# Kernel optimization log

Measured on AMD Instinct MI355X. Metric: run time of the kernel, lower is better.

Reference implementation:

```python
import jax, jax.numpy as jnp
import numpy as np

EPS = 1e-6
B, T, C = 2, 1024, 2048
H, KV, D = 32, 8, 128
E, F, TOPK = 8, 768, 2


def rmsnorm(x, w):
    xf = x.astype(jnp.float32)
    var = jnp.mean(xf * xf, axis=-1, keepdims=True)
    return w * (xf * jax.lax.rsqrt(var + EPS)).astype(x.dtype)


def rotate_half(x):
    d = x.shape[-1] // 2
    return jnp.concatenate([-x[..., d:], x[..., :d]], axis=-1)


def setup_inputs() -> dict:
    key = jax.random.key(0)
    ks = jax.random.split(key, 12)
    sc = 0.02
    x = jax.random.normal(ks[0], (B, T, C), dtype=jnp.float32)
    # RoPE tables: cos/sin of shape [B, T, D]
    inv_freq = 1.0 / (1e6 ** (np.arange(0, D, 2, dtype=np.float32) / D))
    pos = np.arange(T, dtype=np.float32)
    freqs = pos[:, None] * inv_freq[None, :]          # [T, D/2]
    emb = np.concatenate([freqs, freqs], axis=-1)     # [T, D]
    cos = jnp.broadcast_to(jnp.cos(emb)[None], (B, T, D)).astype(jnp.float32)
    sin = jnp.broadcast_to(jnp.sin(emb)[None], (B, T, D)).astype(jnp.float32)
    return {
        "x": x, "cos": cos, "sin": sin,
        "ln1_w": jnp.ones((C,), jnp.float32),
        "q_w": jax.random.normal(ks[1], (C, H * D), jnp.float32) * sc,
        "k_w": jax.random.normal(ks[2], (C, KV * D), jnp.float32) * sc,
        "v_w": jax.random.normal(ks[3], (C, KV * D), jnp.float32) * sc,
        "o_w": jax.random.normal(ks[4], (H * D, C), jnp.float32) * sc,
        "qn_w": jnp.ones((D,), jnp.float32),
        "kn_w": jnp.ones((D,), jnp.float32),
        "ln2_w": jnp.ones((C,), jnp.float32),
        "gate_w": jax.random.normal(ks[5], (C, E), jnp.float32) * sc,
        "gate_up_w": jax.random.normal(ks[6], (E, C, 2 * F), jnp.float32) * sc,
        "down_w": jax.random.normal(ks[7], (E, F, C), jnp.float32) * sc,
    }


def reference(x, cos, sin, ln1_w, q_w, k_w, v_w, o_w, qn_w, kn_w, ln2_w,
              gate_w, gate_up_w, down_w):
    b, t, c = x.shape
    # ---- attention branch ----
    h = rmsnorm(x, ln1_w)
    q = (h @ q_w).reshape(b, t, H, D)
    k = (h @ k_w).reshape(b, t, KV, D)
    v = (h @ v_w).reshape(b, t, KV, D)
    q = rmsnorm(q, qn_w)
    k = rmsnorm(k, kn_w)
    cb = cos[:, :, None, :]
    sb = sin[:, :, None, :]
    q = q * cb + rotate_half(q) * sb
    k = k * cb + rotate_half(k) * sb
    rep = H // KV
    k = jnp.repeat(k, rep, axis=2)  # [b,t,H,D]
    v = jnp.repeat(v, rep, axis=2)
    scores = jnp.einsum('bthd,bshd->bhts', q, k) / jnp.sqrt(jnp.float32(D))
    causal = jnp.tril(jnp.ones((t, t), dtype=bool))
    scores = jnp.where(causal, scores, jnp.finfo(scores.dtype).min)
    attn = jax.nn.softmax(scores, axis=-1)
    ao = jnp.einsum('bhts,bshd->bthd', attn, v).reshape(b, t, H * D) @ o_w
    x = x + ao
    # ---- MoE branch ----
    h2 = rmsnorm(x, ln2_w)
    hidden = h2.reshape(-1, c)                     # [N, C]
    logits = hidden @ gate_w                       # [N, E]
    rw = jax.nn.softmax(logits.astype(jnp.float32), axis=-1)
    tw, ti = jax.lax.top_k(rw, TOPK)
    tw = tw / (tw.sum(axis=-1, keepdims=True) + 1e-9)
    n = hidden.shape[0]
    routed = jnp.zeros_like(logits).at[jnp.arange(n)[:, None], ti].set(tw.astype(logits.dtype))
    routed = routed / (routed.sum(axis=-1, keepdims=True) + 1e-9)
    gu = jnp.einsum('th,ehq->teq', hidden, gate_up_w)   # [N, E, 2F]
    g, u = jnp.split(gu, 2, axis=-1)
    eo = jnp.einsum('teq,eqh->teh', jax.nn.silu(g) * u, down_w)  # [N, E, C]
    moe = (eo * routed[..., None]).sum(axis=1).reshape(b, t, c)
    return x + moe
```

## Files before the change

kernel.cpp:

```cpp
#include <hip/hip_runtime.h>
#include <hip/hip_bf16.h>

typedef short bf16x8 __attribute__((ext_vector_type(8)));
typedef float f32x4 __attribute__((ext_vector_type(4)));
typedef unsigned short u16;

#define NTOK 2048
#define CDIM 2048
#define TSEQ 1024
#define NH   32
#define NKV  8
#define DH   128
#define NE   8
#define FDIM 768
#define CAP  2048

#define GLOAD_LDS16(g, l) \
  __builtin_amdgcn_global_load_lds((const __attribute__((address_space(1))) void*)(g), \
                                   (__attribute__((address_space(3))) void*)(l), 16, 0, 0)

__device__ __forceinline__ u16 f2bf(float f){
  union { float f; unsigned u; } v; v.f = f;
  unsigned r = v.u + 0x7FFFu + ((v.u >> 16) & 1u);
  return (u16)(r >> 16);
}
__device__ __forceinline__ float bf2f(u16 x){
  union { unsigned u; float f; } v; v.u = ((unsigned)x) << 16; return v.f;
}

__device__ __forceinline__ f32x4 mfma_bf16(bf16x8 a, bf16x8 b, f32x4 c){
  return __builtin_amdgcn_mfma_f32_16x16x32_bf16(a, b, c, 0, 0, 0);
}

__device__ __forceinline__ int xcd_swz(int orig, int nwg){
  int xcd = orig & 7;
  int q = nwg >> 3, r = nwg & 7;
  int base = (xcd < r) ? xcd*(q+1) : r*(q+1) + (xcd-r)*q;
  return base + (orig >> 3);
}

__global__ void cast_transpose(const float* __restrict__ in, u16* __restrict__ out,
                               int R, int Cc, int rstride, int d1,
                               long long s_hi, long long s_lo)
{
  __shared__ u16 tile[64][72];
  int z = blockIdx.z;
  in  += (long long)(z / d1) * s_hi + (long long)(z % d1) * s_lo;
  out += (size_t)z * R * Cc;
  int r0 = blockIdx.y*64, c0 = blockIdx.x*64;
  int lr = threadIdx.x >> 4;
  int lc = (threadIdx.x & 15) * 4;
  #pragma unroll
  for(int i=0;i<4;i++){
    int r = lr + i*16;
    float4 v = *(const float4*)(in + (size_t)(r0 + r)*rstride + c0 + lc);
    tile[lc+0][r] = f2bf(v.x);
    tile[lc+1][r] = f2bf(v.y);
    tile[lc+2][r] = f2bf(v.z);
    tile[lc+3][r] = f2bf(v.w);
  }
  __syncthreads();
  int oc  = threadIdx.x >> 2;
  int orr = (threadIdx.x & 3) * 16;
  uint4 a  = *(const uint4*)&tile[oc][orr];
  uint4 b2 = *(const uint4*)&tile[oc][orr + 8];
  *(uint4*)(out + (size_t)(c0+oc)*R + r0 + orr)     = a;
  *(uint4*)(out + (size_t)(c0+oc)*R + r0 + orr + 8) = b2;
}

__global__ void cast_transpose_qkv(const float* __restrict__ qw, const float* __restrict__ kw,
                                   const float* __restrict__ vw, u16* __restrict__ wqkvT)
{
  __shared__ u16 tile[64][72];
  int bx = blockIdx.x;
  const float* in; u16* out; int rstride, c0;
  if(bx < 64){       in = qw; out = wqkvT;                        rstride = 4096; c0 = bx*64; }
  else if(bx < 80){  in = kw; out = wqkvT + (size_t)4096*2048;    rstride = 1024; c0 = (bx-64)*64; }
  else {             in = vw; out = wqkvT + (size_t)5120*2048;    rstride = 1024; c0 = (bx-80)*64; }
  const int R = 2048;
  int r0 = blockIdx.y*64;
  int lr = threadIdx.x >> 4;
  int lc = (threadIdx.x & 15) * 4;
  #pragma unroll
  for(int i=0;i<4;i++){
    int r = lr + i*16;
    float4 v = *(const float4*)(in + (size_t)(r0 + r)*rstride + c0 + lc);
    tile[lc+0][r] = f2bf(v.x);
    tile[lc+1][r] = f2bf(v.y);
    tile[lc+2][r] = f2bf(v.z);
    tile[lc+3][r] = f2bf(v.w);
  }
  __syncthreads();
  int oc  = threadIdx.x >> 2;
  int orr = (threadIdx.x & 3) * 16;
  uint4 a  = *(const uint4*)&tile[oc][orr];
  uint4 b2 = *(const uint4*)&tile[oc][orr + 8];
  *(uint4*)(out + (size_t)(c0+oc)*R + r0 + orr)     = a;
  *(uint4*)(out + (size_t)(c0+oc)*R + r0 + orr + 8) = b2;
}

__global__ void transpose_gate(const float* __restrict__ gw, float* __restrict__ gwT)
{
  int i = blockIdx.x*256 + threadIdx.x;
  int c = i >> 3, e = i & 7;
  gwT[(size_t)e*CDIM + c] = gw[(size_t)c*NE + e];
}

__global__ void transpose_u16(const u16* __restrict__ in, u16* __restrict__ out,
                              int R, int Cc, int rstride, int d1,
                              long long s_hi, long long s_lo)
{
  __shared__ u16 tile[32][34];
  int z = blockIdx.z;
  in += (long long)(z / d1) * s_hi + (long long)(z % d1) * s_lo;
  out += (size_t)z * R * Cc;
  int tx = threadIdx.x & 31, ty = threadIdx.x >> 5;
  int r0 = blockIdx.y * 32, c0 = blockIdx.x * 32;
  #pragma unroll
  for(int i=0;i<4;i++){
    int r = r0 + ty + i*8;
    if(r < R && c0 + tx < Cc) tile[ty + i*8][tx] = in[(size_t)r * rstride + c0 + tx];
  }
  __syncthreads();
  #pragma unroll
  for(int i=0;i<4;i++){
    int c = c0 + ty + i*8;
    if(c < Cc && r0 + tx < R) out[(size_t)c * R + r0 + tx] = tile[tx][ty + i*8];
  }
}

__global__ void rmsnorm_kernel(const float* __restrict__ x, const float* __restrict__ w,
                               u16* __restrict__ outb, float* __restrict__ outf)
{
  __shared__ float sbuf[4];
  int row = blockIdx.x;
  const float* xr = x + (size_t)row * CDIM;
  int t0 = threadIdx.x * 8;
  float4 v0 = *(const float4*)(xr + t0);
  float4 v1 = *(const float4*)(xr + t0 + 4);
  float a[8] = {v0.x,v0.y,v0.z,v0.w,v1.x,v1.y,v1.z,v1.w};
  float ss = 0.f;
  #pragma unroll
  for(int i=0;i<8;i++) ss += a[i]*a[i];
  #pragma unroll
  for(int o=32;o>0;o>>=1) ss += __shfl_xor(ss, o);
  if((threadIdx.x & 63) == 0) sbuf[threadIdx.x >> 6] = ss;
  __syncthreads();
  float tot = sbuf[0]+sbuf[1]+sbuf[2]+sbuf[3];
  float r = rsqrtf(tot * (1.0f/CDIM) + 1e-6f);
  float4 w0 = *(const float4*)(w + t0);
  float4 w1 = *(const float4*)(w + t0 + 4);
  float wv[8] = {w0.x,w0.y,w0.z,w0.w,w1.x,w1.y,w1.z,w1.w};
  #pragma unroll
  for(int i=0;i<8;i++){
    float o = a[i] * r * wv[i];
    outb[(size_t)row*CDIM + t0 + i] = f2bf(o);
    if(outf) outf[(size_t)row*CDIM + t0 + i] = o;
  }
}

__global__ __launch_bounds__(512, 1) void gemm256(const u16* __restrict__ A,
                                                  const u16* __restrict__ Bt,
                                                  u16* __restrict__ Cb,
                                                  int M, int N, int K)
{
  extern __shared__ u16 lds[];
  const int NT = K >> 6;
  int tid = threadIdx.x;
  int lane = tid & 63, g = lane >> 4, cl = lane & 15;
  int wid = tid >> 6, wr = wid >> 2, wc = wid & 3;
  int br = blockIdx.y * 256, bc = blockIdx.x * 192;
  int rowl[4], slotl[4], srcoff[4];
  #pragma unroll
  for(int l=0;l<4;l++){
    int c = l*512 + tid;
    rowl[l]  = c >> 3;
    slotl[l] = c & 7;
    srcoff[l] = (slotl[l] ^ (rowl[l] & 7)) * 8;
  }
  f32x4 acc[8][3];
  #pragma unroll
  for(int m=0;m<8;m++)
    #pragma unroll
    for(int n=0;n<3;n++) acc[m][n] = (f32x4){0.f,0.f,0.f,0.f};

  auto stage = [&](int t, int b){
    int k0 = t << 6;
    #pragma unroll
    for(int l=0;l<4;l++)
      GLOAD_LDS16(A  + (size_t)(br + rowl[l])*K + k0 + srcoff[l],
                  &lds[b*16384 + rowl[l]*64 + slotl[l]*8]);
    #pragma unroll
    for(int l=0;l<3;l++)
      GLOAD_LDS16(Bt + (size_t)(bc + rowl[l])*K + k0 + srcoff[l],
                  &lds[32768 + b*12288 + rowl[l]*64 + slotl[l]*8]);
  };

  stage(0, 0);
  for(int t=0;t<NT;t++){
    int buf = t & 1;
    if(t+1 < NT){
      stage(t+1, buf^1);
      asm volatile("s_waitcnt vmcnt(7)" ::: "memory");
    } else {
      asm volatile("s_waitcnt vmcnt(0)" ::: "memory");
    }
    asm volatile("s_barrier" ::: "memory");
    const u16* As_ = &lds[buf*16384];
    const u16* Bs_ = &lds[32768 + buf*12288];
    __builtin_amdgcn_s_setprio(1);
    #pragma unroll
    for(int kk=0;kk<2;kk++){
      bf16x8 a[8], b[3];
      #pragma unroll
      for(int m=0;m<8;m++){
        int row = wr*128 + m*16 + cl;
        int sl  = ((4*kk + g) ^ (row & 7)) * 8;
        a[m] = *(const bf16x8*)&As_[row*64 + sl];
      }
      #pragma unroll
      for(int n=0;n<3;n++){
        int row = wc*48 + n*16 + cl;
        int sl  = ((4*kk + g) ^ (row & 7)) * 8;
        b[n] = *(const bf16x8*)&Bs_[row*64 + sl];
      }
      #pragma unroll
      for(int m=0;m<8;m++)
        #pragma unroll
        for(int n=0;n<3;n++)
          acc[m][n] = mfma_bf16(a[m], b[n], acc[m][n]);
    }
    __builtin_amdgcn_s_setprio(0);
    asm volatile("s_barrier" ::: "memory");
  }
  #pragma unroll
  for(int m=0;m<8;m++)
    #pragma unroll
    for(int n=0;n<3;n++)
      #pragma unroll
      for(int j=0;j<4;j++){
        int row = br + wr*128 + m*16 + g*4 + j;
        int col = bc + wc*48 + n*16 + cl;
        Cb[(size_t)row*N + col] = f2bf(acc[m][n][j]);
      }
}

__global__ __launch_bounds__(256) void gemm_oproj_pipe(const u16* __restrict__ A,
                                                       const u16* __restrict__ Bt,
                                                       float* __restrict__ C,
                                                       const float* __restrict__ addsrc,
                                                       int M, int N, int K)
{
  extern __shared__ u16 lds[];
  int nwg = gridDim.x;
  int wgid = xcd_swz(blockIdx.x, nwg);
  int nbx = N >> 7;
  int bys = wgid / nbx, bxs = wgid % nbx;
  const int NT = K >> 6;
  int tid = threadIdx.x;
  int lane = tid&63, g = lane>>4, cl = lane&15;
  int w = tid>>6, wr = w>>1, wc = w&1;
  int br = bys*128, bc = bxs*128;
  int rowc[4], slotc[4], srcoff[4];
  #pragma unroll
  for(int l=0;l<4;l++){
    int c = l*256 + tid;
    rowc[l]  = c >> 3;
    slotc[l] = c & 7;
    srcoff[l] = (slotc[l] ^ (rowc[l] & 7)) * 8;
  }
  f32x4 acc[4][4];
  #pragma unroll
  for(int m=0;m<4;m++)
    #pragma unroll
    for(int n=0;n<4;n++) acc[m][n] = (f32x4){0.f,0.f,0.f,0.f};

  auto stage = [&](int t, int b){
    int k0 = t << 6;
    #pragma unroll
    for(int l=0;l<4;l++)
      GLOAD_LDS16(A + (size_t)(br + rowc[l])*K + k0 + srcoff[l],
                  &lds[b*8192 + rowc[l]*64 + slotc[l]*8]);
    #pragma unroll
    for(int l=0;l<4;l++)
      GLOAD_LDS16(Bt + (size_t)(bc + rowc[l])*K + k0 + srcoff[l],
                  &lds[16384 + b*8192 + rowc[l]*64 + slotc[l]*8]);
  };

  stage(0, 0);
  for(int t=0;t<NT;t++){
    int buf = t & 1;
    if(t+1 < NT){
      stage(t+1, buf^1);
      asm volatile("s_waitcnt vmcnt(8)" ::: "memory");
    } else {
      asm volatile("s_waitcnt vmcnt(0)" ::: "memory");
    }
    asm volatile("s_barrier" ::: "memory");
    const u16* As_ = &lds[buf*8192];
    const u16* Bs_ = &lds[16384 + buf*8192];
    __builtin_amdgcn_s_setprio(1);
    #pragma unroll
    for(int kk=0;kk<2;kk++){
      bf16x8 a[4], b[4];
      #pragma unroll
      for(int m=0;m<4;m++){
        int row = wr*64 + m*16 + cl;
        int sl  = ((4*kk + g) ^ (row & 7)) * 8;
        a[m] = *(const bf16x8*)&As_[row*64 + sl];
      }
      #pragma unroll
      for(int n=0;n<4;n++){
        int row = wc*64 + n*16 + cl;
        int sl  = ((4*kk + g) ^ (row & 7)) * 8;
        b[n] = *(const bf16x8*)&Bs_[row*64 + sl];
      }
      #pragma unroll
      for(int m=0;m<4;m++)
        #pragma unroll
        for(int n=0;n<4;n++)
          acc[m][n] = mfma_bf16(a[m], b[n], acc[m][n]);
    }
    __builtin_amdgcn_s_setprio(0);
    asm volatile("s_barrier" ::: "memory");
  }
  #pragma unroll
  for(int m=0;m<4;m++)
    #pragma unroll
    for(int n=0;n<4;n++)
      #pragma unroll
      for(int j=0;j<4;j++){
        int row = br + wr*64 + m*16 + g*4 + j;
        int col = bc + wc*64 + n*16 + cl;
        C[(size_t)row*N + col] = acc[m][n][j] + addsrc[(size_t)row*N + col];
      }
}

__global__ void qk_norm_rope(const u16* __restrict__ qkv, const float* __restrict__ cosb,
                             const float* __restrict__ sinb, const float* __restrict__ qnw,
                             const float* __restrict__ knw,
                             u16* __restrict__ qb, u16* __restrict__ kb)
{
  __shared__ float red[2];
  __shared__ float buf[128];
  int bt = blockIdx.x;
  int head = blockIdx.y;
  int d = threadIdx.x;
  int b = bt >> 10, t = bt & 1023;
  bool isq = head < NH;
  const u16* src = qkv + (size_t)bt*6144 + (isq ? head*DH : 4096 + (head-NH)*DH);
  float v = bf2f(src[d]);
  float ss = v*v;
  #pragma unroll
  for(int o=32;o>0;o>>=1) ss += __shfl_xor(ss, o);
  if((threadIdx.x & 63) == 0) red[threadIdx.x >> 6] = ss;
  __syncthreads();
  float tot = red[0] + red[1];
  float r = rsqrtf(tot * (1.0f/DH) + 1e-6f);
  float nv = v * r * (isq ? qnw[d] : knw[d]);
  buf[d] = nv;
  __syncthreads();
  float rot = (d < 64) ? -buf[d+64] : buf[d-64];
  float cs = cosb[(size_t)bt*DH + d], sn = sinb[(size_t)bt*DH + d];
  float ov = nv*cs + rot*sn;
  if(isq) ov *= 0.08838834764831845f;
  if(isq) qb[(((size_t)b*NH  + head)     *TSEQ + t)*DH + d] = f2bf(ov);
  else    kb[(((size_t)b*NKV + (head-NH))*TSEQ + t)*DH + d] = f2bf(ov);
}

__global__ __launch_bounds__(256) void attn_kernel(const u16* __restrict__ qb,
                                                   const u16* __restrict__ kb,
                                                   const u16* __restrict__ vt,
                                                   u16* __restrict__ aob)
{
  __shared__ u16 Ks[64][136];
  __shared__ u16 Vs[144][72];
  __shared__ u16 Ps[4][32][72];
  int tid = threadIdx.x;
  int w = tid>>6, lane = tid&63, g = lane>>4, cl = lane&15;
  int nwg = gridDim.x * gridDim.y * gridDim.z;
  int orig = (blockIdx.z * gridDim.y + blockIdx.y) * gridDim.x + blockIdx.x;
  int wgid = xcd_swz(orig, nwg);
  int bxs = wgid % gridDim.x;
  int bys = (wgid / gridDim.x) % gridDim.y;
  int bzs = wgid / (gridDim.x * gridDim.y);
  int b = bzs, kvh = bys;
  int qt = (gridDim.x - 1) - bxs;
  int q0 = qt*32;
  int h = kvh*4 + w;
  const u16* qp = qb + (((size_t)b*NH  + h  )*TSEQ)*DH;
  const u16* kp = kb + (((size_t)b*NKV + kvh)*TSEQ)*DH;
  const u16* vp = vt + (((size_t)b*NKV + kvh)*DH)*TSEQ;
  for(int idx = tid; idx < 16*72; idx += 256){
    int r = idx / 72, c2 = idx % 72;
    Vs[128 + r][c2] = (r == 0) ? (u16)0x3F80 : (u16)0;
  }
  bf16x8 aq[2][4];
  #pragma unroll
  for(int m=0;m<2;m++)
    #pragma unroll
    for(int kd=0;kd<4;kd++)
      aq[m][kd] = *(const bf16x8*)(qp + (size_t)(q0 + m*16 + cl)*DH + kd*32 + g*8);
  f32x4 accO[2][9];
  #pragma unroll
  for(int m=0;m<2;m++)
    #pragma unroll
    for(int n=0;n<9;n++) accO[m][n] = (f32x4){0.f,0.f,0.f,0.f};
  float mr[2][4];
  #pragma unroll
  for(int m=0;m<2;m++)
    #pragma unroll
    for(int j=0;j<4;j++) mr[m][j] = -1e30f;
  for(int kv0 = 0; kv0 < q0 + 32; kv0 += 64){
    #pragma unroll
    for(int it=0; it<4; it++){
      int c = tid + it*256;
      int kr = c>>4, kcol = (c&15)*8;
      *(uint4*)&Ks[kr][kcol] = *(const uint4*)(kp + (size_t)(kv0 + kr)*DH + kcol);
      int vr = c>>3, vcol = (c&7)*8;
      *(uint4*)&Vs[vr][vcol] = *(const uint4*)(vp + (size_t)vr*TSEQ + kv0 + vcol);
    }
    __syncthreads();
    f32x4 sc[2][4];
    #pragma unroll
    for(int m=0;m<2;m++)
      #pragma unroll
      for(int n=0;n<4;n++) sc[m][n] = (f32x4){0.f,0.f,0.f,0.f};
    __builtin_amdgcn_s_setprio(1);
    #pragma unroll
    for(int kd=0;kd<4;kd++){
      bf16x8 bk[4];
      #pragma unroll
      for(int n=0;n<4;n++) bk[n] = *(const bf16x8*)&Ks[n*16 + cl][kd*32 + g*8];
      #pragma unroll
      for(int m=0;m<2;m++)
        #pragma unroll
        for(int n=0;n<4;n++)
          sc[m][n] = mfma_bf16(aq[m][kd], bk[n], sc[m][n]);
    }
    __builtin_amdgcn_s_setprio(0);
    if(kv0 + 63 > q0){
      #pragma unroll
      for(int m=0;m<2;m++)
        #pragma unroll
        for(int n=0;n<4;n++)
          #pragma unroll
          for(int j=0;j<4;j++){
            int row = q0 + m*16 + g*4 + j;
            int col = kv0 + n*16 + cl;
            if(col > row) sc[m][n][j] = -1e30f;
          }
    }
    float tmax[2][4];
    #pragma unroll
    for(int m=0;m<2;m++)
      #pragma unroll
      for(int j=0;j<4;j++)
        tmax[m][j] = fmaxf(fmaxf(sc[m][0][j], sc[m][1][j]), fmaxf(sc[m][2][j], sc[m][3][j]));
    #pragma unroll
    for(int o=1;o<16;o<<=1)
      #pragma unroll
      for(int m=0;m<2;m++)
        #pragma unroll
        for(int j=0;j<4;j++) tmax[m][j] = fmaxf(tmax[m][j], __shfl_xor(tmax[m][j], o));
    float grow = -1e30f;
    #pragma unroll
    for(int m=0;m<2;m++)
      #pragma unroll
      for(int j=0;j<4;j++) grow = fmaxf(grow, tmax[m][j] - mr[m][j]);
    grow = fmaxf(grow, __shfl_xor(grow, 16));
    grow = fmaxf(grow, __shfl_xor(grow, 32));
    if(grow > 8.0f){
      #pragma unroll
      for(int m=0;m<2;m++)
        #pragma unroll
        for(int j=0;j<4;j++){
          float mn = fmaxf(mr[m][j], tmax[m][j]);
          float f  = __expf(mr[m][j] - mn);
          mr[m][j] = mn;
          #pragma unroll
          for(int n=0;n<9;n++) accO[m][n][j] *= f;
        }
    }
    #pragma unroll
    for(int m=0;m<2;m++)
      #pragma unroll
      for(int n=0;n<4;n++)
        #pragma unroll
        for(int j=0;j<4;j++)
          sc[m][n][j] = __expf(sc[m][n][j] - mr[m][j]);
    #pragma unroll
    for(int m=0;m<2;m++)
      #pragma unroll
      for(int n=0;n<4;n++)
        #pragma unroll
        for(int j=0;j<4;j++)
          Ps[w][m*16 + g*4 + j][n*16 + cl] = f2bf(sc[m][n][j]);
    bf16x8 pa[2][2];
    #pragma unroll
    for(int m=0;m<2;m++)
      #pragma unroll
      for(int s2=0;s2<2;s2++)
        pa[m][s2] = *(const bf16x8*)&Ps[w][m*16 + cl][s2*32 + g*8];
    __builtin_amdgcn_s_setprio(1);
    #pragma unroll
    for(int n=0;n<9;n++){
      #pragma unroll
      for(int s2=0;s2<2;s2++){
        bf16x8 bv = *(const bf16x8*)&Vs[n*16 + cl][s2*32 + g*8];
        #pragma unroll
        for(int m=0;m<2;m++)
          accO[m][n] = mfma_bf16(pa[m][s2], bv, accO[m][n]);
      }
    }
    __builtin_amdgcn_s_setprio(0);
    __syncthreads();
  }
  #pragma unroll
  for(int m=0;m<2;m++){
    float linv[4];
    #pragma unroll
    for(int j=0;j<4;j++){
      float l = __shfl(accO[m][8][j], lane & 48);
      linv[j] = 1.0f / l;
    }
    #pragma unroll
    for(int n=0;n<8;n++)
      #pragma unroll
      for(int j=0;j<4;j++){
        int row = q0 + m*16 + g*4 + j;
        float v = accO[m][n][j] * linv[j];
        aob[((size_t)b*TSEQ + row)*(NH*DH) + h*DH + n*16 + cl] = f2bf(v);
      }
  }
}

__global__ void route_kernel(const float* __restrict__ h2f, const float* __restrict__ gwT,
                             int* __restrict__ cnt, int* __restrict__ bidx,
                             float* __restrict__ bw)
{
  int lane = threadIdx.x & 63;
  int token = blockIdx.x*4 + (threadIdx.x >> 6);
  float acc[8];
  #pragma unroll
  for(int e=0;e<8;e++) acc[e]=0.f;
  for(int c0 = lane*4; c0 < CDIM; c0 += 256){
    float4 hv = *(const float4*)(h2f + (size_t)token*CDIM + c0);
    #pragma unroll
    for(int e=0;e<8;e++){
      float4 gv = *(const float4*)(gwT + (size_t)e*CDIM + c0);
      acc[e] += hv.x*gv.x + hv.y*gv.y + hv.z*gv.z + hv.w*gv.w;
    }
  }
  #pragma unroll
  for(int o=32;o>0;o>>=1)
    #pragma unroll
    for(int e=0;e<8;e++) acc[e] += __shfl_xor(acc[e], o);
  if(lane==0){
    float mx = acc[0];
    #pragma unroll
    for(int e=1;e<8;e++) mx = fmaxf(mx, acc[e]);
    float rw[8]; float s=0.f;
    #pragma unroll
    for(int e=0;e<8;e++){ rw[e] = __expf(acc[e]-mx); s += rw[e]; }
    #pragma unroll
    for(int e=0;e<8;e++) rw[e] /= s;
    int i0=0;
    #pragma unroll
    for(int e=1;e<8;e++) if(rw[e] > rw[i0]) i0=e;
    int i1 = (i0==0)?1:0;
    #pragma unroll
    for(int e=0;e<8;e++) if(e!=i0 && rw[e] > rw[i1]) i1=e;
    float tw0=rw[i0], tw1=rw[i1];
    float s1 = tw0+tw1+1e-9f;
    float a0 = tw0/s1, a1 = tw1/s1;
    float s2 = a0+a1+1e-9f;
    float w0 = a0/s2, w1 = a1/s2;
    int sl0 = atomicAdd(&cnt[i0],1);
    bidx[i0*CAP + sl0] = token; bw[i0*CAP + sl0] = w0;
    int sl1 = atomicAdd(&cnt[i1],1);
    bidx[i1*CAP + sl1] = token; bw[i1*CAP + sl1] = w1;
  }
}

__global__ __launch_bounds__(256) void gemm_gateup_pipe(const u16* __restrict__ h2b,
                                                        const u16* __restrict__ gupT,
                                                        u16* __restrict__ act,
                                                        const int* __restrict__ bidx,
                                                        const int* __restrict__ cnt)
{
  extern __shared__ u16 lds[];
  int d = blockIdx.x;
  int e = d & 7, j = d >> 3;
  int y = j / 6, x = j % 6;
  int nc = cnt[e];
  int sr = y*128;
  if(sr >= nc) return;
  const int K = CDIM, NT = K >> 6;
  const u16* Btg = gupT + (size_t)e*1536*CDIM + (size_t)(x*128)*CDIM;
  const u16* Btu = Btg + (size_t)768*CDIM;
  const int* be = bidx + e*CAP;
  int tid = threadIdx.x;
  int lane = tid&63, g = lane>>4, cl = lane&15;
  int w = tid>>6, wr = w>>1, wc = w&1;
  int rowc[4], slotc[4], srcoff[4];
  long long atok[4];
  #pragma unroll
  for(int l=0;l<4;l++){
    int c = l*256 + tid;
    rowc[l]  = c >> 3;
    slotc[l] = c & 7;
    srcoff[l] = (slotc[l] ^ (rowc[l] & 7)) * 8;
    int t = be[sr + rowc[l]];
    if(t < 0 || t >= NTOK) t = 0;
    atok[l] = (long long)t * CDIM;
  }
  f32x4 accG[4][4], accU[4][4];
  #pragma unroll
  for(int m=0;m<4;m++)
    #pragma unroll
    for(int n=0;n<4;n++){ accG[m][n] = (f32x4){0.f,0.f,0.f,0.f}; accU[m][n] = (f32x4){0.f,0.f,0.f,0.f}; }

  auto stage = [&](int t, int b){
    int k0 = t << 6;
    #pragma unroll
    for(int l=0;l<4;l++)
      GLOAD_LDS16(h2b + atok[l] + k0 + srcoff[l],
                  &lds[b*8192 + rowc[l]*64 + slotc[l]*8]);
    #pragma unroll
    for(int l=0;l<4;l++)
      GLOAD_LDS16(Btg + (size_t)rowc[l]*K + k0 + srcoff[l],
                  &lds[16384 + b*8192 + rowc[l]*64 + slotc[l]*8]);
    #pragma unroll
    for(int l=0;l<4;l++)
      GLOAD_LDS16(Btu + (size_t)rowc[l]*K + k0 + srcoff[l],
                  &lds[32768 + b*8192 + rowc[l]*64 + slotc[l]*8]);
  };

  stage(0, 0);
  for(int t=0;t<NT;t++){
    int buf = t & 1;
    if(t+1 < NT){
      stage(t+1, buf^1);
      asm volatile("s_waitcnt vmcnt(12)" ::: "memory");
    } else {
      asm volatile("s_waitcnt vmcnt(0)" ::: "memory");
    }
    asm volatile("s_barrier" ::: "memory");
    const u16* As_ = &lds[buf*8192];
    const u16* Bg_ = &lds[16384 + buf*8192];
    const u16* Bu_ = &lds[32768 + buf*8192];
    __builtin_amdgcn_s_setprio(1);
    #pragma unroll
    for(int kk=0;kk<2;kk++){
      bf16x8 a[4], bg[4], bu[4];
      #pragma unroll
      for(int m=0;m<4;m++){
        int row = wr*64 + m*16 + cl;
        int sl  = ((4*kk + g) ^ (row & 7)) * 8;
        a[m] = *(const bf16x8*)&As_[row*64 + sl];
      }
      #pragma unroll
      for(int n=0;n<4;n++){
        int row = wc*64 + n*16 + cl;
        int sl  = ((4*kk + g) ^ (row & 7)) * 8;
        bg[n] = *(const bf16x8*)&Bg_[row*64 + sl];
        bu[n] = *(const bf16x8*)&Bu_[row*64 + sl];
      }
      #pragma unroll
      for(int m=0;m<4;m++)
        #pragma unroll
        for(int n=0;n<4;n++){
          accG[m][n] = mfma_bf16(a[m], bg[n], accG[m][n]);
          accU[m][n] = mfma_bf16(a[m], bu[n], accU[m][n]);
        }
    }
    __builtin_amdgcn_s_setprio(0);
    asm volatile("s_barrier" ::: "memory");
  }
  #pragma unroll
  for(int m=0;m<4;m++)
    #pragma unroll
    for(int n=0;n<4;n++)
      #pragma unroll
      for(int jj=0;jj<4;jj++){
        int slot = sr + wr*64 + m*16 + g*4 + jj;
        int col  = x*128 + wc*64 + n*16 + cl;
        float gv = accG[m][n][jj], uv = accU[m][n][jj];
        float av = gv / (1.f + __expf(-gv)) * uv;
        act[((size_t)e*CAP + slot)*FDIM + col] = f2bf(av);
      }
}

__global__ __launch_bounds__(256) void gemm_down_pipe(const u16* __restrict__ act,
                                                      const u16* __restrict__ downT,
                                                      float* __restrict__ out,
                                                      const int* __restrict__ bidx,
                                                      const float* __restrict__ bw,
                                                      const int* __restrict__ cnt)
{
  extern __shared__ u16 lds[];
  int d = blockIdx.x;
  int e = d & 7, j = d >> 3;
  int y = j >> 4, x = j & 15;
  int nc = cnt[e];
  int sr = y*128;
  if(sr >= nc) return;
  const int K = FDIM, NT = K >> 6;
  const u16* A  = act   + ((size_t)e*CAP + sr)*FDIM;
  const u16* Bt = downT + (size_t)e*CDIM*FDIM + (size_t)(x*128)*FDIM;
  const int* be = bidx + e*CAP;
  const float* bwe = bw + e*CAP;
  int tid = threadIdx.x;
  int lane = tid&63, g = lane>>4, cl = lane&15;
  int w = tid>>6, wr = w>>1, wc = w&1;
  int rowc[4], slotc[4], srcoff[4];
  #pragma unroll
  for(int l=0;l<4;l++){
    int c = l*256 + tid;
    rowc[l]  = c >> 3;
    slotc[l] = c & 7;
    srcoff[l] = (slotc[l] ^ (rowc[l] & 7)) * 8;
  }
  f32x4 acc[4][4];
  #pragma unroll
  for(int m=0;m<4;m++)
    #pragma unroll
    for(int n=0;n<4;n++) acc[m][n] = (f32x4){0.f,0.f,0.f,0.f};

  auto stage = [&](int t, int b){
    int k0 = t << 6;
    #pragma unroll
    for(int l=0;l<4;l++)
      GLOAD_LDS16(A + (size_t)rowc[l]*K + k0 + srcoff[l],
                  &lds[b*8192 + rowc[l]*64 + slotc[l]*8]);
    #pragma unroll
    for(int l=0;l<4;l++)
      GLOAD_LDS16(Bt + (size_t)rowc[l]*K + k0 + srcoff[l],
                  &lds[16384 + b*8192 + rowc[l]*64 + slotc[l]*8]);
  };

  stage(0, 0);
  for(int t=0;t<NT;t++){
    int buf = t & 1;
    if(t+1 < NT){
      stage(t+1, buf^1);
      asm volatile("s_waitcnt vmcnt(8)" ::: "memory");
    } else {
      asm volatile("s_waitcnt vmcnt(0)" ::: "memory");
    }
    asm volatile("s_barrier" ::: "memory");
    const u16* As_ = &lds[buf*8192];
    const u16* Bs_ = &lds[16384 + buf*8192];
    __builtin_amdgcn_s_setprio(1);
    #pragma unroll
    for(int kk=0;kk<2;kk++){
      bf16x8 a[4], b[4];
      #pragma unroll
      for(int m=0;m<4;m++){
        int row = wr*64 + m*16 + cl;
        int sl  = ((4*kk + g) ^ (row & 7)) * 8;
        a[m] = *(const bf16x8*)&As_[row*64 + sl];
      }
      #pragma unroll
      for(int n=0;n<4;n++){
        int row = wc*64 + n*16 + cl;
        int sl  = ((4*kk + g) ^ (row & 7)) * 8;
        b[n] = *(const bf16x8*)&Bs_[row*64 + sl];
      }
      #pragma unroll
      for(int m=0;m<4;m++)
        #pragma unroll
        for(int n=0;n<4;n++)
          acc[m][n] = mfma_bf16(a[m], b[n], acc[m][n]);
    }
    __builtin_amdgcn_s_setprio(0);
    asm volatile("s_barrier" ::: "memory");
  }
  #pragma unroll
  for(int m=0;m<4;m++)
    #pragma unroll
    for(int jj=0;jj<4;jj++){
      int slot = sr + wr*64 + m*16 + g*4 + jj;
      if(slot < nc){
        int tok = be[slot];
        float wgt = bwe[slot];
        #pragma unroll
        for(int n=0;n<4;n++){
          int col = x*128 + wc*64 + n*16 + cl;
          atomicAdd(out + (size_t)tok*CDIM + col, wgt * acc[m][n][jj]);
        }
      }
    }
}

extern "C" void kernel_launch(void* const* d_in, const int* in_sizes, int n_in,
                              void* d_out, int out_size, void* d_ws, size_t ws_size,
                              hipStream_t stream)
{
  const float* x     = (const float*)d_in[0];
  const float* cosb  = (const float*)d_in[1];
  const float* sinb  = (const float*)d_in[2];
  const float* ln1w  = (const float*)d_in[3];
  const float* qw    = (const float*)d_in[4];
  const float* kw    = (const float*)d_in[5];
  const float* vw    = (const float*)d_in[6];
  const float* ow    = (const float*)d_in[7];
  const float* qnw   = (const float*)d_in[8];
  const float* knw   = (const float*)d_in[9];
  const float* ln2w  = (const float*)d_in[10];
  const float* gatew = (const float*)d_in[11];
  const float* gupw  = (const float*)d_in[12];
  const float* downw = (const float*)d_in[13];
  float* out = (float*)d_out;

  char* ws = (char*)d_ws;
  size_t off = 0;
  auto alloc = [&](size_t bytes)->char*{
    char* p = ws + off;
    off = (off + bytes + 255) & ~(size_t)255;
    return p;
  };
  u16*   wqkvT = (u16*)  alloc((size_t)6144*2048*2);
  u16*   owT   = (u16*)  alloc((size_t)2048*4096*2);
  u16*   gupT  = (u16*)  alloc((size_t)8*1536*2048*2);
  u16*   downT = (u16*)  alloc((size_t)8*2048*768*2);
  u16*   h1b   = (u16*)  alloc((size_t)2048*2048*2);
  u16*   qkvb  = (u16*)  alloc((size_t)2048*6144*2);
  u16*   qb    = (u16*)  alloc((size_t)2*32*1024*128*2);
  u16*   kb    = (u16*)  alloc((size_t)2*8*1024*128*2);
  u16*   vt    = (u16*)  alloc((size_t)2*8*1024*128*2);
  u16*   aob   = (u16*)  alloc((size_t)2048*4096*2);
  float* h2f   = (float*)alloc((size_t)2048*2048*4);
  u16*   h2b   = (u16*)  alloc((size_t)2048*2048*2);
  u16*   actb  = (u16*)  alloc((size_t)8*2048*768*2);
  int*   bidx  = (int*)  alloc((size_t)8*2048*4);
  float* bwgt  = (float*)alloc((size_t)8*2048*4);
  float* gwT   = (float*)alloc((size_t)8*2048*4);
  int*   cnt   = (int*)  alloc(64);
  (void)ws_size; (void)in_sizes; (void)n_in; (void)out_size;

  hipMemsetAsync(cnt, 0, 8*sizeof(int), stream);

  cast_transpose_qkv<<<dim3(96,32), 256, 0, stream>>>(qw, kw, vw, wqkvT);
  cast_transpose<<<dim3(32,64,1), 256, 0, stream>>>(ow, owT,      4096, 2048, 2048, 1, 0, 0);
  cast_transpose<<<dim3(24,32,8), 256, 0, stream>>>(gupw, gupT,   2048, 1536, 1536, 8, 0, (long long)2048*1536);
  cast_transpose<<<dim3(32,12,8), 256, 0, stream>>>(downw, downT, 768,  2048, 2048, 8, 0, (long long)768*2048);
  transpose_gate<<<64, 256, 0, stream>>>(gatew, gwT);

  rmsnorm_kernel<<<2048, 256, 0, stream>>>(x, ln1w, h1b, nullptr);
  gemm256<<<dim3(32,8), 512, 114688, stream>>>(h1b, wqkvT, qkvb, 2048, 6144, 2048);
  qk_norm_rope<<<dim3(2048,40), 128, 0, stream>>>(qkvb, cosb, sinb, qnw, knw, qb, kb);
  transpose_u16<<<dim3(4,32,16), 256, 0, stream>>>(qkvb + 5120, vt, 1024, 128, 6144, 8,
                                                   (long long)1024*6144, 128);
  attn_kernel<<<dim3(32,8,2), 256, 0, stream>>>(qb, kb, vt, aob);
  gemm_oproj_pipe<<<256, 256, 65536, stream>>>(aob, owT, out, x, 2048, 2048, 4096);
  rmsnorm_kernel<<<2048, 256, 0, stream>>>(out, ln2w, h2b, h2f);
  route_kernel<<<512, 256, 0, stream>>>(h2f, gwT, cnt, bidx, bwgt);
  gemm_gateup_pipe<<<768, 256, 98304, stream>>>(h2b, gupT, actb, bidx, cnt);
  gemm_down_pipe<<<2048, 256, 65536, stream>>>(actb, downT, out, bidx, bwgt, cnt);
}
```

Before: 462.4 us.

## Split long causal attention tiles across two KV halves with combine kernel

Query tiles in the second half of the sequence now process their KV range as two independent blocks, each writing unnormalized fp32 partial outputs plus row max and sum. A new combine kernel rescales and merges the two partials into the bf16 attention output. This evens out per-block work under the causal mask and raises block count, at the cost of extra partial-buffer traffic, an extra launch, and the loss of the XCD-aware block swizzle.

```diff
diff --git a/kernel.cpp b/kernel.cpp
--- a/kernel.cpp
+++ b/kernel.cpp
@@ -371,22 +371,38 @@
 __global__ __launch_bounds__(256) void attn_kernel(const u16* __restrict__ qb,
                                                    const u16* __restrict__ kb,
                                                    const u16* __restrict__ vt,
-                                                   u16* __restrict__ aob)
+                                                   u16* __restrict__ aob,
+                                                   float* __restrict__ pO,
+                                                   float* __restrict__ pml)
 {
   __shared__ u16 Ks[64][136];
   __shared__ u16 Vs[144][72];
   __shared__ u16 Ps[4][32][72];
   int tid = threadIdx.x;
   int w = tid>>6, lane = tid&63, g = lane>>4, cl = lane&15;
-  int nwg = gridDim.x * gridDim.y * gridDim.z;
-  int orig = (blockIdx.z * gridDim.y + blockIdx.y) * gridDim.x + blockIdx.x;
-  int wgid = xcd_swz(orig, nwg);
-  int bxs = wgid % gridDim.x;
-  int bys = (wgid / gridDim.x) % gridDim.y;
-  int bzs = wgid / (gridDim.x * gridDim.y);
-  int b = bzs, kvh = bys;
-  int qt = (gridDim.x - 1) - bxs;
+  int bid = blockIdx.x;
+  int t3 = bid / 3, r3 = bid % 3;
+  int b, kvh, qt, half; bool split;
+  if(r3 < 2){
+    split = true;
+    int hidx = t3*2 + r3;
+    b = hidx >> 8;
+    int rem = hidx & 255;
+    kvh = rem >> 5;
+    int rem2 = rem & 31;
+    qt = 16 + (rem2 >> 1);
+    half = rem2 & 1;
+  } else {
+    split = false; half = 0;
+    int lidx = t3;
+    b = lidx >> 7;
+    int rem = lidx & 127;
+    kvh = rem >> 4;
+    qt = rem & 15;
+  }
   int q0 = qt*32;
+  int kvs   = (split && half) ? 512 : 0;
+  int kvend = (split && !half) ? 512 : (q0 + 32);
   int h = kvh*4 + w;
   const u16* qp = qb + (((size_t)b*NH  + h  )*TSEQ)*DH;
   const u16* kp = kb + (((size_t)b*NKV + kvh)*TSEQ)*DH;
@@ -411,7 +427,7 @@
   for(int m=0;m<2;m++)
     #pragma unroll
     for(int j=0;j<4;j++) mr[m][j] = -1e30f;
-  for(int kv0 = 0; kv0 < q0 + 32; kv0 += 64){
+  for(int kv0 = kvs; kv0 < kvend; kv0 += 64){
     #pragma unroll
     for(int it=0; it<4; it++){
       int c = tid + it*256;
@@ -516,23 +532,60 @@
     __builtin_amdgcn_s_setprio(0);
     __syncthreads();
   }
-  #pragma unroll
-  for(int m=0;m<2;m++){
-    float linv[4];
-    #pragma unroll
-    for(int j=0;j<4;j++){
-      float l = __shfl(accO[m][8][j], lane & 48);
-      linv[j] = 1.0f / l;
-    }
-    #pragma unroll
-    for(int n=0;n<8;n++)
+  if(!split){
+    #pragma unroll
+    for(int m=0;m<2;m++){
+      float linv[4];
+      #pragma unroll
+      for(int j=0;j<4;j++){
+        float l = __shfl(accO[m][8][j], lane & 48);
+        linv[j] = 1.0f / l;
+      }
+      #pragma unroll
+      for(int n=0;n<8;n++)
+        #pragma unroll
+        for(int j=0;j<4;j++){
+          int row = q0 + m*16 + g*4 + j;
+          float v = accO[m][n][j] * linv[j];
+          aob[((size_t)b*TSEQ + row)*(NH*DH) + h*DH + n*16 + cl] = f2bf(v);
+        }
+    }
+  } else {
+    #pragma unroll
+    for(int m=0;m<2;m++)
       #pragma unroll
       for(int j=0;j<4;j++){
         int row = q0 + m*16 + g*4 + j;
-        float v = accO[m][n][j] * linv[j];
-        aob[((size_t)b*TSEQ + row)*(NH*DH) + h*DH + n*16 + cl] = f2bf(v);
-      }
-  }
+        int rr = row - 512;
+        size_t pb = (((size_t)half*2 + b)*NH + h)*512 + rr;
+        #pragma unroll
+        for(int n=0;n<8;n++)
+          pO[pb*128 + n*16 + cl] = accO[m][n][j];
+        if(cl == 0){
+          pml[pb*2]     = mr[m][j];
+          pml[pb*2 + 1] = accO[m][8][j];
+        }
+      }
+  }
+}
+
+__global__ void attn_combine(const float* __restrict__ pO, const float* __restrict__ pml,
+                             u16* __restrict__ aob)
+{
+  int rr = blockIdx.x;
+  int h  = blockIdx.y;
+  int b  = blockIdx.z;
+  int d  = threadIdx.x;
+  size_t p0 = (((size_t)0*2 + b)*NH + h)*512 + rr;
+  size_t p1 = (((size_t)1*2 + b)*NH + h)*512 + rr;
+  float m0 = pml[p0*2], l0 = pml[p0*2 + 1];
+  float m1 = pml[p1*2], l1 = pml[p1*2 + 1];
+  float M  = fmaxf(m0, m1);
+  float w0 = __expf(m0 - M), w1 = __expf(m1 - M);
+  float denom = l0*w0 + l1*w1;
+  float v = (pO[p0*128 + d]*w0 + pO[p1*128 + d]*w1) / denom;
+  int row = 512 + rr;
+  aob[((size_t)b*TSEQ + row)*(NH*DH) + h*DH + d] = f2bf(v);
 }
 
 __global__ void route_kernel(const float* __restrict__ h2f, const float* __restrict__ gwT,
@@ -837,6 +890,8 @@
   int*   bidx  = (int*)  alloc((size_t)8*2048*4);
   float* bwgt  = (float*)alloc((size_t)8*2048*4);
   float* gwT   = (float*)alloc((size_t)8*2048*4);
+  float* pO    = (float*)alloc((size_t)2*2*32*512*128*4);
+  float* pml   = (float*)alloc((size_t)2*2*32*512*2*4);
   int*   cnt   = (int*)  alloc(64);
   (void)ws_size; (void)in_sizes; (void)n_in; (void)out_size;
 
@@ -853,7 +908,8 @@
   qk_norm_rope<<<dim3(2048,40), 128, 0, stream>>>(qkvb, cosb, sinb, qnw, knw, qb, kb);
   transpose_u16<<<dim3(4,32,16), 256, 0, stream>>>(qkvb + 5120, vt, 1024, 128, 6144, 8,
                                                    (long long)1024*6144, 128);
-  attn_kernel<<<dim3(32,8,2), 256, 0, stream>>>(qb, kb, vt, aob);
+  attn_kernel<<<768, 256, 0, stream>>>(qb, kb, vt, aob, pO, pml);
+  attn_combine<<<dim3(512,32,2), 128, 0, stream>>>(pO, pml, aob);
   gemm_oproj_pipe<<<256, 256, 65536, stream>>>(aob, owT, out, x, 2048, 2048, 4096);
   rmsnorm_kernel<<<2048, 256, 0, stream>>>(out, ln2w, h2b, h2f);
   route_kernel<<<512, 256, 0, stream>>>(h2f, gwT, cnt, bidx, bwgt);
```

Result: slower. 492.8 us (+6.6%).
